# Kernel tuning notes

Measured on AMD Instinct MI355X. Metric: run time of the kernel, lower is better.

Reference implementation:

```python
import jax, jax.numpy as jnp
import numpy as np

NH = 12   # heads
KD = 64   # key_dim = dim // heads


def setup_inputs() -> dict:
    key = jax.random.key(0)
    ks = jax.random.split(key, 6)
    B, N, C = 64, 1024, 768
    qkv_out = (1 + 2 * KD) * NH  # 1548
    s = 0.02
    return {
        "x": jax.random.normal(ks[0], (B, N, C), dtype=jnp.float32),
        "w_qkv": jax.random.normal(ks[1], (qkv_out, C), dtype=jnp.float32) * s,
        "b_qkv": jax.random.normal(ks[2], (qkv_out,), dtype=jnp.float32) * s,
        "w_cv": jax.random.normal(ks[3], (1, N), dtype=jnp.float32) * s,
        "w_out": jax.random.normal(ks[4], (C, C), dtype=jnp.float32) * s,
        "b_out": jax.random.normal(ks[5], (C,), dtype=jnp.float32) * s,
    }


def reference(x, w_qkv, b_qkv, w_cv, w_out, b_out):
    B, N, C = x.shape
    # qkv projection: [B, N, (1+2*KD)*NH] -> [B, N, NH, 1+2*KD]
    qkv = (jnp.einsum("bnc,oc->bno", x, w_qkv) + b_qkv).reshape(B, N, NH, 1 + 2 * KD)
    q = qkv[..., :1]                 # [B, N, NH, 1]
    k = qkv[..., 1:1 + KD]           # [B, N, NH, KD]
    v = qkv[..., 1 + KD:]            # [B, N, NH, KD]
    # softmax pooling over the token axis N (dropout p=0 -> identity)
    scores = jax.nn.softmax(q, axis=1)          # [B, N, NH, 1]
    # cv_proj: Linear(token_len -> 1), no bias, applied over token axis
    cv = jnp.einsum("bnhd,n->bhd", k * scores, w_cv[0])  # [B, NH, KD]
    # gated ReLU: relu(value) * broadcast context vector
    out = jax.nn.relu(v) * cv[:, None, :, :]    # [B, N, NH, KD]
    out = out.reshape(B, N, NH * KD)
    return jnp.einsum("bnc,oc->bno", out, w_out) + b_out
```

## Files before the change

kernel.cpp:

```cpp
#include <hip/hip_runtime.h>
#include <hip/hip_bf16.h>

typedef unsigned short u16;
typedef __attribute__((ext_vector_type(8))) short bf16x8;
typedef __attribute__((ext_vector_type(8))) unsigned short u16x8;
typedef __attribute__((ext_vector_type(4))) float f32x4;

#define NHh 12
#define KDd 64
#define Bb 64
#define Nn 1024
#define Cc 768
#define Oo 1548
#define Mm 65536

__device__ __forceinline__ float bf2f(u16 u) {
    union { unsigned int i; float f; } x; x.i = ((unsigned int)u) << 16; return x.f;
}
__device__ __forceinline__ u16 f2bf(float f) {
    union { float f; unsigned int i; } x; x.f = f;
    unsigned int r = x.i + 0x7fffu + ((x.i >> 16) & 1u);
    return (u16)(r >> 16);
}
__device__ __forceinline__ unsigned int cvtpk(float a, float b) {
    unsigned int r;
    asm("v_cvt_pk_bf16_f32 %0, %1, %2" : "=v"(r) : "v"(a), "v"(b));
    return r;
}

__device__ __forceinline__ void async16(const u16* g, u16* l) {
    __builtin_amdgcn_global_load_lds(
        (const __attribute__((address_space(1))) void*)g,
        (__attribute__((address_space(3))) void*)l, 16, 0, 0);
}

__global__ void detect_kernel(const u16* __restrict__ w, int* __restrict__ flag)
{
    __shared__ int cnt;
    if (threadIdx.x == 0) cnt = 0;
    __syncthreads();
    int c = 0;
#pragma unroll
    for (int i = 0; i < 4; ++i) {
        const u16 u = w[(threadIdx.x * 4 + i) * 2];
        const int e = (u >> 7) & 0xFF;
        c += ((e >= 0x60 && e <= 0x9F) || u == 0) ? 1 : 0;
    }
    atomicAdd(&cnt, c);
    __syncthreads();
    if (threadIdx.x == 0) flag[0] = (cnt >= 160) ? 1 : 0;
}

__global__ __launch_bounds__(256) void cvt_kernel(
    const float* __restrict__ src, u16* __restrict__ dst, int n16,
    const int* __restrict__ flagp)
{
    if (flagp[0]) return;
    const int i = blockIdx.x * 256 + threadIdx.x;
    if (i >= n16) return;
    const float* p = src + (size_t)i * 16;
    const f32x4 a0 = *(const f32x4*)p;
    const f32x4 a1 = *(const f32x4*)(p + 4);
    const f32x4 a2 = *(const f32x4*)(p + 8);
    const f32x4 a3 = *(const f32x4*)(p + 12);
    union { unsigned int u[8]; u16x8 v[2]; } pk;
    pk.u[0] = cvtpk(a0[0], a0[1]); pk.u[1] = cvtpk(a0[2], a0[3]);
    pk.u[2] = cvtpk(a1[0], a1[1]); pk.u[3] = cvtpk(a1[2], a1[3]);
    pk.u[4] = cvtpk(a2[0], a2[1]); pk.u[5] = cvtpk(a2[2], a2[3]);
    pk.u[6] = cvtpk(a3[0], a3[1]); pk.u[7] = cvtpk(a3[2], a3[3]);
    *(u16x8*)(dst + (size_t)i * 16)     = pk.v[0];
    *(u16x8*)(dst + (size_t)i * 16 + 8) = pk.v[1];
}

template <int EPI>
__global__ __launch_bounds__(512, 2) void gemm_bt(
    const void* __restrict__ Aorig, const u16* __restrict__ Acvt,
    const void* __restrict__ Borig, const u16* __restrict__ Bcvt,
    const void* __restrict__ biasv, const int* __restrict__ flagp,
    int Nout, int K, int lda, int ldb, int ntn,
    float* __restrict__ Qf, u16* __restrict__ Kb, u16* __restrict__ Vb,
    u16* __restrict__ Cout16, float* __restrict__ Cout32, int ldc)
{
    __shared__ __align__(16) u16 lA2[2 * 256 * 64];
    __shared__ __align__(16) u16 lB2[2 * 128 * 64];

    const int isbf = flagp[0];
    const u16* A  = isbf ? (const u16*)Aorig : Acvt;
    const u16* Bp = isbf ? (const u16*)Borig : Bcvt;

    const int t = threadIdx.x;
    const int lane = t & 63, wave = t >> 6;

    int bid = blockIdx.x;
    {
        const int nwg = (int)gridDim.x;
        const int cpx = nwg >> 3;
        bid = (bid & 7) * cpx + (bid >> 3);
    }
    const int tm = bid / ntn, tn = bid % ntn;
    const int m0 = tm * 256, o0 = tn * 128;

    const int srow = t >> 3;
    const int scol = (t & 7) * 8;
    const int ssw  = (((t & 7) ^ (srow & 7)) * 8);

    const int wr = wave >> 1, wc = wave & 1;
    const int R0 = wr * 64, C0 = wc * 64;
    const int lr = lane & 15, lq = lane >> 4;
    const int sw8 = lr & 7;

    const u16* aSrc[4];
    const u16* bSrc[2];
#pragma unroll
    for (int i = 0; i < 4; ++i)
        aSrc[i] = A + (size_t)(m0 + i * 64 + srow) * lda + ssw;
#pragma unroll
    for (int i = 0; i < 2; ++i) {
        int o = o0 + i * 64 + srow;
        if (o > Nout - 1) o = Nout - 1;
        bSrc[i] = Bp + (size_t)o * ldb + ssw;
    }

    f32x4 acc[4][4];
    const f32x4 zero = {0.f, 0.f, 0.f, 0.f};
#pragma unroll
    for (int i = 0; i < 4; ++i)
#pragma unroll
        for (int j = 0; j < 4; ++j) acc[i][j] = zero;

    auto STAGE = [&](int kt, int buf) {
        const int k0 = kt * 64;
        u16* la = &lA2[buf * (256 * 64)];
        u16* lb = &lB2[buf * (128 * 64)];
#pragma unroll
        for (int i = 0; i < 4; ++i)
            async16(aSrc[i] + k0, &la[(i * 64 + srow) * 64 + scol]);
#pragma unroll
        for (int i = 0; i < 2; ++i)
            async16(bSrc[i] + k0, &lb[(i * 64 + srow) * 64 + scol]);
    };

    const int NT = K >> 6;
    STAGE(0, 0);
    asm volatile("s_waitcnt vmcnt(0)" ::: "memory");
    __builtin_amdgcn_s_barrier();
    __builtin_amdgcn_sched_barrier(0);

    for (int kt = 0; kt < NT; ++kt) {
        const int cur = kt & 1;
        if (kt + 1 < NT) STAGE(kt + 1, cur ^ 1);
        __builtin_amdgcn_sched_barrier(0);

        const u16* la = &lA2[cur * (256 * 64)];
        const u16* lb = &lB2[cur * (128 * 64)];
        __builtin_amdgcn_s_setprio(1);
#pragma unroll
        for (int kk = 0; kk < 2; ++kk) {
            bf16x8 af[4], bfr[4];
            const int sl = (((kk * 4 + lq) ^ sw8) * 8);
#pragma unroll
            for (int i = 0; i < 4; ++i)
                af[i] = *(const bf16x8*)&la[(R0 + i * 16 + lr) * 64 + sl];
#pragma unroll
            for (int j = 0; j < 4; ++j)
                bfr[j] = *(const bf16x8*)&lb[(C0 + j * 16 + lr) * 64 + sl];
#pragma unroll
            for (int i = 0; i < 4; ++i)
#pragma unroll
                for (int j = 0; j < 4; ++j)
                    acc[i][j] = __builtin_amdgcn_mfma_f32_16x16x32_bf16(af[i], bfr[j], acc[i][j], 0, 0, 0);
        }
        __builtin_amdgcn_s_setprio(0);
        __builtin_amdgcn_sched_barrier(0);
        asm volatile("s_waitcnt vmcnt(0)" ::: "memory");
        __builtin_amdgcn_s_barrier();
    }

#pragma unroll
    for (int i = 0; i < 4; ++i) {
#pragma unroll
        for (int j = 0; j < 4; ++j) {
            const int ob = o0 + C0 + j * 16 + lr;
            float bv = 0.f;
            if (ob < Nout)
                bv = isbf ? bf2f(((const u16*)biasv)[ob]) : ((const float*)biasv)[ob];
#pragma unroll
            for (int r = 0; r < 4; ++r) {
                const int row = m0 + R0 + i * 16 + lq * 4 + r;
                const float val = acc[i][j][r] + bv;
                if (EPI == 1) {
                    if (ob < Nout) {
                        const int h = ob / 129;
                        const int rr = ob - h * 129;
                        const size_t mh = (size_t)row * 12 + h;
                        if (rr == 0)       Qf[mh] = val;
                        else if (rr <= 64) Kb[mh * 64 + (rr - 1)]  = f2bf(val);
                        else               Vb[mh * 64 + (rr - 65)] = f2bf(val);
                    }
                } else {
                    if (isbf) Cout16[(size_t)row * ldc + ob] = f2bf(val);
                    else      Cout32[(size_t)row * ldc + ob] = val;
                }
            }
        }
    }
}

__global__ __launch_bounds__(256) void softmax_cv_kernel(
    const float* __restrict__ Qf, const u16* __restrict__ Kb,
    const void* __restrict__ wcvv, const int* __restrict__ flagp,
    float* __restrict__ cv)
{
    const int isbf = flagp[0];
    const int bh = blockIdx.x;
    const int b = bh / NHh, h = bh - (bh / NHh) * NHh;
    const int t = threadIdx.x;

    __shared__ float sp[1024];
    __shared__ float red[256];
    __shared__ float redd[64 * 33];

    float q[4];
#pragma unroll
    for (int i = 0; i < 4; ++i) {
        const int n = t + i * 256;
        q[i] = Qf[(size_t)(b * Nn + n) * NHh + h];
    }
    float mx = fmaxf(fmaxf(q[0], q[1]), fmaxf(q[2], q[3]));
    red[t] = mx; __syncthreads();
    for (int off = 128; off; off >>= 1) {
        if (t < off) red[t] = fmaxf(red[t], red[t + off]);
        __syncthreads();
    }
    mx = red[0];
    __syncthreads();

    float sloc = 0.f;
#pragma unroll
    for (int i = 0; i < 4; ++i) {
        const int n = t + i * 256;
        const float e = __expf(q[i] - mx);
        sloc += e;
        const float wv = isbf ? bf2f(((const u16*)wcvv)[n]) : ((const float*)wcvv)[n];
        sp[n] = e * wv;
    }
    red[t] = sloc; __syncthreads();
    for (int off = 128; off; off >>= 1) {
        if (t < off) red[t] += red[t + off];
        __syncthreads();
    }
    const float s = red[0];
    __syncthreads();

    const int dt8 = (t & 7) * 8;
    const int ng  = t >> 3;
    float a8[8];
#pragma unroll
    for (int i = 0; i < 8; ++i) a8[i] = 0.f;
    const u16* Kbase = Kb + ((size_t)b * Nn * NHh + h) * 64 + dt8;
#pragma unroll 4
    for (int it = 0; it < 32; ++it) {
        const int n = it * 32 + ng;
        const u16x8 kv = *(const u16x8*)(Kbase + (size_t)n * 768);
        const float p = sp[n];
#pragma unroll
        for (int i = 0; i < 8; ++i) a8[i] = fmaf(bf2f(kv[i]), p, a8[i]);
    }
#pragma unroll
    for (int i = 0; i < 8; ++i) redd[(dt8 + i) * 33 + ng] = a8[i];
    __syncthreads();
    if (t < 64) {
        float tot = 0.f;
#pragma unroll 8
        for (int g2 = 0; g2 < 32; ++g2) tot += redd[t * 33 + g2];
        cv[(size_t)bh * 64 + t] = tot / s;
    }
}

__global__ __launch_bounds__(256) void relu_cv_kernel(
    u16* __restrict__ Vb, const float* __restrict__ cv)
{
    const size_t idx = ((size_t)blockIdx.x * 256 + threadIdx.x) * 8;
    const int c = (int)(idx % 768);
    const size_t m = idx / 768;
    const int b = (int)(m >> 10);
    const int h = c >> 6, d0 = c & 63;
    const float* cvp = cv + ((size_t)b * NHh + h) * 64 + d0;

    u16x8 r = *(const u16x8*)(Vb + idx);
#pragma unroll
    for (int i = 0; i < 8; ++i) {
        const float f = fmaxf(bf2f(r[i]), 0.f) * cvp[i];
        r[i] = f2bf(f);
    }
    *(u16x8*)(Vb + idx) = r;
}

extern "C" void kernel_launch(void* const* d_in, const int* in_sizes, int n_in,
                              void* d_out, int out_size, void* d_ws, size_t ws_size,
                              hipStream_t stream)
{
    const void* x     = d_in[0];
    const void* w_qkv = d_in[1];
    const void* b_qkv = d_in[2];
    const void* w_cv  = d_in[3];
    const void* w_out = d_in[4];
    const void* b_out = d_in[5];

    char* w = (char*)d_ws;
    float* Qf = (float*)w;
    u16*   Kb = (u16*)(w + 3145728);
    u16*   Vb = (u16*)(w + 3145728 + 100663296);
    float* cv = (float*)(w + 3145728 + 2ll * 100663296);
    int* flag = (int*)(w + 3145728 + 2ll * 100663296 + 196608);
    u16* wqkvb = (u16*)(w + 3145728 + 2ll * 100663296 + 196608 + 4096);
    u16* woutb = (u16*)((char*)wqkvb + 2377728);

    u16* xb = (u16*)d_out;

    detect_kernel<<<1, 64, 0, stream>>>((const u16*)w_qkv, flag);

    cvt_kernel<<<(Mm * Cc) / (256 * 16), 256, 0, stream>>>((const float*)x, xb, (Mm * Cc) / 16, flag);
    cvt_kernel<<<(Oo * Cc + 256 * 16 - 1) / (256 * 16), 256, 0, stream>>>((const float*)w_qkv, wqkvb, (Oo * Cc) / 16, flag);
    cvt_kernel<<<(Cc * Cc) / (256 * 16), 256, 0, stream>>>((const float*)w_out, woutb, (Cc * Cc) / 16, flag);

    gemm_bt<1><<<256 * 13, 512, 0, stream>>>(x, xb, w_qkv, wqkvb, b_qkv, flag,
        Oo, Cc, Cc, Cc, 13, Qf, Kb, Vb, nullptr, nullptr, 0);

    softmax_cv_kernel<<<Bb * NHh, 256, 0, stream>>>(Qf, Kb, w_cv, flag, cv);

    relu_cv_kernel<<<(Mm * 768) / (256 * 8), 256, 0, stream>>>(Vb, cv);

    gemm_bt<2><<<256 * 6, 512, 0, stream>>>(Vb, (const u16*)Vb, w_out, woutb, b_out, flag,
        Cc, Cc, Cc, Cc, 6, nullptr, nullptr, nullptr, (u16*)d_out, (float*)d_out, Cc);
}
```

Baseline: 899.6 us.

## Shrink GEMM tiles to 128x128x32, fuse relu-gate into softmax, merge conversions

Several changes land together. The GEMM moves from 256x128 tiles with K-step 64 on 512 threads to 128x128 tiles with K-step 32 on 256 threads and 4 blocks per CU, with a new LDS swizzle and the epilogue head index hoisted out of the row loop. The relu-times-cv gating is fused into the softmax/cv kernel, so one launch and a global cv round trip go away. The three fp32-to-bf16 conversion launches are merged into one kernel. Smaller tiles lower per-block LDS and may raise occupancy, but they cut operand reuse and double the number of K iterations and barriers.

```diff
diff --git a/kernel.cpp b/kernel.cpp
--- a/kernel.cpp
+++ b/kernel.cpp
@@ -51,14 +51,12 @@
     if (threadIdx.x == 0) flag[0] = (cnt >= 160) ? 1 : 0;
 }
 
-__global__ __launch_bounds__(256) void cvt_kernel(
-    const float* __restrict__ src, u16* __restrict__ dst, int n16,
-    const int* __restrict__ flagp)
-{
-    if (flagp[0]) return;
-    const int i = blockIdx.x * 256 + threadIdx.x;
-    if (i >= n16) return;
-    const float* p = src + (size_t)i * 16;
+#define NX16 3145728
+#define NQ16 74304
+#define NO16 36864
+
+__device__ __forceinline__ void cvt16(const float* p, u16* d)
+{
     const f32x4 a0 = *(const f32x4*)p;
     const f32x4 a1 = *(const f32x4*)(p + 4);
     const f32x4 a2 = *(const f32x4*)(p + 8);
@@ -68,12 +66,31 @@
     pk.u[2] = cvtpk(a1[0], a1[1]); pk.u[3] = cvtpk(a1[2], a1[3]);
     pk.u[4] = cvtpk(a2[0], a2[1]); pk.u[5] = cvtpk(a2[2], a2[3]);
     pk.u[6] = cvtpk(a3[0], a3[1]); pk.u[7] = cvtpk(a3[2], a3[3]);
-    *(u16x8*)(dst + (size_t)i * 16)     = pk.v[0];
-    *(u16x8*)(dst + (size_t)i * 16 + 8) = pk.v[1];
+    *(u16x8*)d       = pk.v[0];
+    *(u16x8*)(d + 8) = pk.v[1];
+}
+
+__global__ __launch_bounds__(256) void cvt3_kernel(
+    const float* __restrict__ x,  u16* __restrict__ xb,
+    const float* __restrict__ wq, u16* __restrict__ wqb,
+    const float* __restrict__ wo, u16* __restrict__ wob,
+    const int* __restrict__ flagp)
+{
+    if (flagp[0]) return;
+    const int i = blockIdx.x * 256 + threadIdx.x;
+    if (i < NX16) {
+        cvt16(x + (size_t)i * 16, xb + (size_t)i * 16);
+    } else if (i < NX16 + NQ16) {
+        const int j = i - NX16;
+        cvt16(wq + (size_t)j * 16, wqb + (size_t)j * 16);
+    } else if (i < NX16 + NQ16 + NO16) {
+        const int j = i - NX16 - NQ16;
+        cvt16(wo + (size_t)j * 16, wob + (size_t)j * 16);
+    }
 }
 
 template <int EPI>
-__global__ __launch_bounds__(512, 2) void gemm_bt(
+__global__ __launch_bounds__(256, 4) void gemm_bt(
     const void* __restrict__ Aorig, const u16* __restrict__ Acvt,
     const void* __restrict__ Borig, const u16* __restrict__ Bcvt,
     const void* __restrict__ biasv, const int* __restrict__ flagp,
@@ -81,8 +98,8 @@
     float* __restrict__ Qf, u16* __restrict__ Kb, u16* __restrict__ Vb,
     u16* __restrict__ Cout16, float* __restrict__ Cout32, int ldc)
 {
-    __shared__ __align__(16) u16 lA2[2 * 256 * 64];
-    __shared__ __align__(16) u16 lB2[2 * 128 * 64];
+    __shared__ __align__(16) u16 lA2[2 * 128 * 32];
+    __shared__ __align__(16) u16 lB2[2 * 128 * 32];
 
     const int isbf = flagp[0];
     const u16* A  = isbf ? (const u16*)Aorig : Acvt;
@@ -98,28 +115,24 @@
         bid = (bid & 7) * cpx + (bid >> 3);
     }
     const int tm = bid / ntn, tn = bid % ntn;
-    const int m0 = tm * 256, o0 = tn * 128;
-
-    const int srow = t >> 3;
-    const int scol = (t & 7) * 8;
-    const int ssw  = (((t & 7) ^ (srow & 7)) * 8);
-
-    const int wr = wave >> 1, wc = wave & 1;
-    const int R0 = wr * 64, C0 = wc * 64;
+    const int m0 = tm * 128, o0 = tn * 128;
+
+    const int srow = t >> 2;
+    const int scc  = t & 3;
+    const int ssw  = (scc ^ ((srow ^ (srow >> 2)) & 3)) * 8;
+    const int sdst = t * 8;
+
+    const int R0 = (wave >> 1) * 64, C0 = (wave & 1) * 64;
     const int lr = lane & 15, lq = lane >> 4;
-    const int sw8 = lr & 7;
-
-    const u16* aSrc[4];
-    const u16* bSrc[2];
-#pragma unroll
-    for (int i = 0; i < 4; ++i)
-        aSrc[i] = A + (size_t)(m0 + i * 64 + srow) * lda + ssw;
-#pragma unroll
-    for (int i = 0; i < 2; ++i) {
-        int o = o0 + i * 64 + srow;
-        if (o > Nout - 1) o = Nout - 1;
-        bSrc[i] = Bp + (size_t)o * ldb + ssw;
-    }
+    const int sw2 = (lr ^ (lr >> 2)) & 3;
+    const int sl  = (lq ^ sw2) * 8;
+
+    const u16* aS0 = A + (size_t)(m0 + srow) * lda + ssw;
+    const u16* aS1 = A + (size_t)(m0 + 64 + srow) * lda + ssw;
+    int ob0 = o0 + srow;      if (ob0 > Nout - 1) ob0 = Nout - 1;
+    int ob1 = o0 + 64 + srow; if (ob1 > Nout - 1) ob1 = Nout - 1;
+    const u16* bS0 = Bp + (size_t)ob0 * ldb + ssw;
+    const u16* bS1 = Bp + (size_t)ob1 * ldb + ssw;
 
     f32x4 acc[4][4];
     const f32x4 zero = {0.f, 0.f, 0.f, 0.f};
@@ -129,18 +142,16 @@
         for (int j = 0; j < 4; ++j) acc[i][j] = zero;
 
     auto STAGE = [&](int kt, int buf) {
-        const int k0 = kt * 64;
-        u16* la = &lA2[buf * (256 * 64)];
-        u16* lb = &lB2[buf * (128 * 64)];
-#pragma unroll
-        for (int i = 0; i < 4; ++i)
-            async16(aSrc[i] + k0, &la[(i * 64 + srow) * 64 + scol]);
-#pragma unroll
-        for (int i = 0; i < 2; ++i)
-            async16(bSrc[i] + k0, &lb[(i * 64 + srow) * 64 + scol]);
+        const int k0 = kt * 32;
+        u16* la = &lA2[buf * (128 * 32)];
+        u16* lb = &lB2[buf * (128 * 32)];
+        async16(aS0 + k0, &la[sdst]);
+        async16(aS1 + k0, &la[sdst + 64 * 32]);
+        async16(bS0 + k0, &lb[sdst]);
+        async16(bS1 + k0, &lb[sdst + 64 * 32]);
     };
 
-    const int NT = K >> 6;
+    const int NT = K >> 5;
     STAGE(0, 0);
     asm volatile("s_waitcnt vmcnt(0)" ::: "memory");
     __builtin_amdgcn_s_barrier();
@@ -151,19 +162,17 @@
         if (kt + 1 < NT) STAGE(kt + 1, cur ^ 1);
         __builtin_amdgcn_sched_barrier(0);
 
-        const u16* la = &lA2[cur * (256 * 64)];
-        const u16* lb = &lB2[cur * (128 * 64)];
+        const u16* la = &lA2[cur * (128 * 32)];
+        const u16* lb = &lB2[cur * (128 * 32)];
         __builtin_amdgcn_s_setprio(1);
-#pragma unroll
-        for (int kk = 0; kk < 2; ++kk) {
+        {
             bf16x8 af[4], bfr[4];
-            const int sl = (((kk * 4 + lq) ^ sw8) * 8);
 #pragma unroll
             for (int i = 0; i < 4; ++i)
-                af[i] = *(const bf16x8*)&la[(R0 + i * 16 + lr) * 64 + sl];
+                af[i] = *(const bf16x8*)&la[(R0 + i * 16 + lr) * 32 + sl];
 #pragma unroll
             for (int j = 0; j < 4; ++j)
-                bfr[j] = *(const bf16x8*)&lb[(C0 + j * 16 + lr) * 64 + sl];
+                bfr[j] = *(const bf16x8*)&lb[(C0 + j * 16 + lr) * 32 + sl];
 #pragma unroll
             for (int i = 0; i < 4; ++i)
 #pragma unroll
@@ -177,21 +186,23 @@
     }
 
 #pragma unroll
-    for (int i = 0; i < 4; ++i) {
-#pragma unroll
-        for (int j = 0; j < 4; ++j) {
-            const int ob = o0 + C0 + j * 16 + lr;
-            float bv = 0.f;
-            if (ob < Nout)
-                bv = isbf ? bf2f(((const u16*)biasv)[ob]) : ((const float*)biasv)[ob];
+    for (int j = 0; j < 4; ++j) {
+        const int ob = o0 + C0 + j * 16 + lr;
+        const bool valid = (ob < Nout);
+        float bv = 0.f;
+        int h = 0, rr = 0;
+        if (valid) {
+            bv = isbf ? bf2f(((const u16*)biasv)[ob]) : ((const float*)biasv)[ob];
+            if (EPI == 1) { h = ob / 129; rr = ob - h * 129; }
+        }
+#pragma unroll
+        for (int i = 0; i < 4; ++i) {
 #pragma unroll
             for (int r = 0; r < 4; ++r) {
                 const int row = m0 + R0 + i * 16 + lq * 4 + r;
                 const float val = acc[i][j][r] + bv;
                 if (EPI == 1) {
-                    if (ob < Nout) {
-                        const int h = ob / 129;
-                        const int rr = ob - h * 129;
+                    if (valid) {
                         const size_t mh = (size_t)row * 12 + h;
                         if (rr == 0)       Qf[mh] = val;
                         else if (rr <= 64) Kb[mh * 64 + (rr - 1)]  = f2bf(val);
@@ -208,8 +219,8 @@
 
 __global__ __launch_bounds__(256) void softmax_cv_kernel(
     const float* __restrict__ Qf, const u16* __restrict__ Kb,
-    const void* __restrict__ wcvv, const int* __restrict__ flagp,
-    float* __restrict__ cv)
+    u16* __restrict__ Vb,
+    const void* __restrict__ wcvv, const int* __restrict__ flagp)
 {
     const int isbf = flagp[0];
     const int bh = blockIdx.x;
@@ -219,6 +230,7 @@
     __shared__ float sp[1024];
     __shared__ float red[256];
     __shared__ float redd[64 * 33];
+    __shared__ float cvs[64];
 
     float q[4];
 #pragma unroll
@@ -273,27 +285,25 @@
         float tot = 0.f;
 #pragma unroll 8
         for (int g2 = 0; g2 < 32; ++g2) tot += redd[t * 33 + g2];
-        cv[(size_t)bh * 64 + t] = tot / s;
-    }
-}
-
-__global__ __launch_bounds__(256) void relu_cv_kernel(
-    u16* __restrict__ Vb, const float* __restrict__ cv)
-{
-    const size_t idx = ((size_t)blockIdx.x * 256 + threadIdx.x) * 8;
-    const int c = (int)(idx % 768);
-    const size_t m = idx / 768;
-    const int b = (int)(m >> 10);
-    const int h = c >> 6, d0 = c & 63;
-    const float* cvp = cv + ((size_t)b * NHh + h) * 64 + d0;
-
-    u16x8 r = *(const u16x8*)(Vb + idx);
-#pragma unroll
-    for (int i = 0; i < 8; ++i) {
-        const float f = fmaxf(bf2f(r[i]), 0.f) * cvp[i];
-        r[i] = f2bf(f);
-    }
-    *(u16x8*)(Vb + idx) = r;
+        cvs[t] = tot / s;
+    }
+    __syncthreads();
+
+    float c8[8];
+#pragma unroll
+    for (int i = 0; i < 8; ++i) c8[i] = cvs[dt8 + i];
+    u16* Vp = Vb + ((size_t)b * Nn * NHh + h) * 64 + dt8;
+#pragma unroll 4
+    for (int it = 0; it < 32; ++it) {
+        const int n = it * 32 + ng;
+        u16x8 r = *(u16x8*)(Vp + (size_t)n * 768);
+#pragma unroll
+        for (int i = 0; i < 8; ++i) {
+            const float f = fmaxf(bf2f(r[i]), 0.f) * c8[i];
+            r[i] = f2bf(f);
+        }
+        *(u16x8*)(Vp + (size_t)n * 768) = r;
+    }
 }
 
 extern "C" void kernel_launch(void* const* d_in, const int* in_sizes, int n_in,
@@ -311,7 +321,6 @@
     float* Qf = (float*)w;
     u16*   Kb = (u16*)(w + 3145728);
     u16*   Vb = (u16*)(w + 3145728 + 100663296);
-    float* cv = (float*)(w + 3145728 + 2ll * 100663296);
     int* flag = (int*)(w + 3145728 + 2ll * 100663296 + 196608);
     u16* wqkvb = (u16*)(w + 3145728 + 2ll * 100663296 + 196608 + 4096);
     u16* woutb = (u16*)((char*)wqkvb + 2377728);
@@ -320,17 +329,14 @@
 
     detect_kernel<<<1, 64, 0, stream>>>((const u16*)w_qkv, flag);
 
-    cvt_kernel<<<(Mm * Cc) / (256 * 16), 256, 0, stream>>>((const float*)x, xb, (Mm * Cc) / 16, flag);
-    cvt_kernel<<<(Oo * Cc + 256 * 16 - 1) / (256 * 16), 256, 0, stream>>>((const float*)w_qkv, wqkvb, (Oo * Cc) / 16, flag);
-    cvt_kernel<<<(Cc * Cc) / (256 * 16), 256, 0, stream>>>((const float*)w_out, woutb, (Cc * Cc) / 16, flag);
-
-    gemm_bt<1><<<256 * 13, 512, 0, stream>>>(x, xb, w_qkv, wqkvb, b_qkv, flag,
+    cvt3_kernel<<<(NX16 + NQ16 + NO16 + 255) / 256, 256, 0, stream>>>(
+        (const float*)x, xb, (const float*)w_qkv, wqkvb, (const float*)w_out, woutb, flag);
+
+    gemm_bt<1><<<512 * 13, 256, 0, stream>>>(x, xb, w_qkv, wqkvb, b_qkv, flag,
         Oo, Cc, Cc, Cc, 13, Qf, Kb, Vb, nullptr, nullptr, 0);
 
-    softmax_cv_kernel<<<Bb * NHh, 256, 0, stream>>>(Qf, Kb, w_cv, flag, cv);
-
-    relu_cv_kernel<<<(Mm * 768) / (256 * 8), 256, 0, stream>>>(Vb, cv);
-
-    gemm_bt<2><<<256 * 6, 512, 0, stream>>>(Vb, (const u16*)Vb, w_out, woutb, b_out, flag,
+    softmax_cv_kernel<<<Bb * NHh, 256, 0, stream>>>(Qf, Kb, Vb, w_cv, flag);
+
+    gemm_bt<2><<<512 * 6, 256, 0, stream>>>(Vb, (const u16*)Vb, w_out, woutb, b_out, flag,
         Cc, Cc, Cc, Cc, 6, nullptr, nullptr, nullptr, (u16*)d_out, (float*)d_out, Cc);
 }
```

Result: faster. 804.6 us (-10.6%).
